# Performance work log

Hardware: AMD Instinct MI355X
Metric: run time of the kernel (lower is better)

Reference implementation:

```python
import jax, jax.numpy as jnp
import numpy as np
jax.config.update("jax_enable_x64", True)  # int64 hash codes for lattice keys

N_KPTS = 32768
C = 61      # feature channels; f-MLP input dim is C+3 = 64
D = 64      # disp-distribution channels
D_LAT = 8   # last f-layer output -> permutohedral position dim

# large odd 62-bit multipliers for the lattice-key hash (wraps mod 2^64)
_MULTS = np.array([2654435761405764093, 1181783497276652981,
                   3202034522624059733, 2685821657736338717,
                   1876998521354586173, 1481765933965188213,
                   2549297995355413921, 3373259426345127233], dtype=np.int64)


def _hcode(k, mults):
    return jnp.sum(k.astype(jnp.int64) * mults, axis=-1)


def _pl_filter(pos, vals):
    """Permutohedral lattice splat -> blur -> slice (approx. Gaussian filter).
    pos: (N, d) float32 lattice positions, vals: (N, vd) float32 values."""
    N, d = pos.shape
    vd = vals.shape[1]
    M = N * (d + 1)  # fixed-size hash table (every point touches d+1 vertices)
    # --- elevate onto hyperplane H_d in R^{d+1} ---
    scale = np.float32(np.sqrt(2.0 / 3.0) * (d + 1)) / np.sqrt(
        np.arange(1, d + 1, dtype=np.float32) * np.arange(2, d + 2, dtype=np.float32))
    E = np.zeros((d + 1, d), dtype=np.float32)
    E[0, :] = 1.0
    for i in range(1, d + 1):
        E[i, i - 1] = -float(i)
        E[i, i:] = 1.0
    elevated = (pos * jnp.asarray(scale, jnp.float32)) @ jnp.asarray(E).T  # (N, d+1)
    # --- nearest zero-colored lattice point and simplex ranks ---
    rem0 = jnp.floor(elevated / (d + 1) + 0.5) * (d + 1)
    sum_val = jnp.round(jnp.sum(rem0, -1) / (d + 1)).astype(jnp.int32)
    diff = elevated - rem0
    rank = jnp.argsort(jnp.argsort(-diff, axis=-1), axis=-1).astype(jnp.int32) + sum_val[:, None]
    lo = rank < 0
    hi = rank > d
    rem0 = rem0 + jnp.where(lo, float(d + 1), 0.0) - jnp.where(hi, float(d + 1), 0.0)
    rank = rank + jnp.where(lo, d + 1, 0) - jnp.where(hi, d + 1, 0)
    # --- barycentric coordinates ---
    t = (elevated - rem0) / (d + 1)
    rows = jnp.arange(N)[:, None]
    bary = jnp.zeros((N, d + 2), jnp.float32)
    bary = bary.at[rows, d - rank].add(t)
    bary = bary.at[rows, d + 1 - rank].add(-t)
    bary = bary.at[:, 0].add(1.0 + bary[:, d + 1])
    w = bary[:, :d + 1]  # (N, d+1) vertex weights
    # --- simplex vertex keys (first d coords; full key sums to 0) ---
    canonical = np.zeros((d + 1, d + 1), np.int32)
    for r in range(d + 1):
        canonical[r, :d + 1 - r] = r
        canonical[r, d + 1 - r:] = r - (d + 1)
    keys = rem0.astype(jnp.int32)[None, :, :d] + jnp.asarray(canonical)[:, rank[:, :d]]  # (d+1,N,d)
    # --- hash table via sorted unique codes (jit-safe fixed size) ---
    mults = jnp.asarray(_MULTS[:d])
    codes = _hcode(keys, mults).reshape(M)
    uniq, inv = jnp.unique(codes, return_inverse=True, size=M,
                           fill_value=jnp.iinfo(jnp.int64).max)
    inv = inv.reshape(M)
    # --- splat ---
    wv = (w.T[:, :, None] * vals[None]).reshape(M, vd)
    lat = jax.ops.segment_sum(wv, inv, num_segments=M)  # (M, vd)
    occ = jax.ops.segment_sum(jnp.ones((M,), jnp.float32), inv, num_segments=M) > 0
    ukeys = jnp.zeros((M, d), jnp.int32).at[inv].set(keys.reshape(M, d))
    # --- blur along each of the d+1 lattice directions ---
    for j in range(d + 1):
        off = np.ones(d + 1, np.int32)
        off[j] = -d
        o = jnp.asarray(off[:d])
        def _nbr(sign, lat=lat):
            c = _hcode(ukeys + sign * o, mults)
            i = jnp.clip(jnp.searchsorted(uniq, c), 0, M - 1)
            ok = (jnp.take(uniq, i) == c) & jnp.take(occ, i)
            return jnp.where(ok[:, None], jnp.take(lat, i, axis=0), 0.0)
        lat = jnp.where(occ[:, None], 0.5 * lat + 0.25 * (_nbr(1) + _nbr(-1)), lat)
    # --- slice ---
    alpha = 1.0 / (1.0 + 2.0 ** (-d))
    return jnp.sum(w.T[:, :, None] * jnp.take(lat, inv, axis=0).reshape(d + 1, N, vd), 0) * alpha


def _layernorm2(x, g, b):
    # LayerNorm(normalized_shape=(N, K)): stats over the last TWO dims jointly
    mu = jnp.mean(x, axis=(-2, -1), keepdims=True)
    var = jnp.mean((x - mu) ** 2, axis=(-2, -1), keepdims=True)
    return (x - mu) * jax.lax.rsqrt(var + 1e-5) * g + b


def setup_inputs() -> dict:
    key = jax.random.key(0)
    ks = jax.random.split(key, 16)
    f32 = jnp.float32
    rn = lambda k, shape, s=1.0: jax.random.normal(k, shape, dtype=f32) * s
    inp = {
        "kpts": rn(ks[0], (1, N_KPTS, 3)),
        "disps_distr": rn(ks[1], (1, N_KPTS, D)),
        "feats": rn(ks[2], (1, N_KPTS, C)),
    }
    i = 3
    for b in range(2):
        inp[f"Wd{b}0"] = rn(ks[i], (D, D), 0.05); i += 1
        inp[f"bd{b}0"] = jnp.zeros((D,), f32)
        inp[f"Wd{b}1"] = rn(ks[i], (D, D), 0.05); i += 1
        inp[f"bd{b}1"] = jnp.zeros((D,), f32)
        inp[f"Wf{b}"] = rn(ks[i], (C + 3, D_LAT), 0.1); i += 1
        inp[f"bf{b}"] = jnp.zeros((D_LAT,), f32)
        inp[f"g{b}"] = jnp.ones((N_KPTS, D_LAT), f32)
        inp[f"be{b}"] = jnp.zeros((N_KPTS, D_LAT), f32)
    return inp


def reference(kpts, disps_distr, feats, Wd00, bd00, Wd01, bd01, Wf0, bf0, g0, be0,
              Wd10, bd10, Wd11, bd11, Wf1, bf1, g1, be1):
    fk = jnp.concatenate([kpts, feats], axis=-1)  # (1, N, C+3)
    x = jnp.reshape(disps_distr, (1, N_KPTS, -1))
    blocks = [(Wd00, bd00, Wd01, bd01, Wf0, bf0, g0, be0),
              (Wd10, bd10, Wd11, bd11, Wf1, bf1, g1, be1)]
    for (Wd0, bd0, Wd1, bd1, Wf, bf, g, be) in blocks:
        x = jax.nn.relu(x @ Wd0 + bd0)   # d-layer 0
        x = jax.nn.relu(x @ Wd1 + bd1)   # d-layer 1
        # only the LAST f-layer output is used by the torch code (feats_kpts is never updated)
        pos = _layernorm2(jax.nn.relu(fk @ Wf + bf), g, be)  # (1, N, 8)
        x = _pl_filter(pos[0], x[0])[None]
    return x
```

## Files before the change

kernel.cpp:

```cpp
#include <hip/hip_runtime.h>
#include <hip/hip_bf16.h>
#include <hip/hip_fp16.h>
#include <stdint.h>

typedef unsigned long long u64;

#define NK 32768
#define DL 8
#define DP1 9
#define MT (NK*DP1)
#define HBITS 20
#define HSIZE (1u<<HBITS)
#define HMASK (HSIZE-1)
#define EMPTY_CODE 0xFFFFFFFFFFFFFFFFULL
#define NBLK 1152
#define HBLK 4096
#define CAP 32

__device__ __constant__ u64 c_mults[8] = {
    2654435761405764093ULL, 1181783497276652981ULL, 3202034522624059733ULL,
    2685821657736338717ULL, 1876998521354586173ULL, 1481765933965188213ULL,
    2549297995355413921ULL, 3373259426345127233ULL};

__device__ __forceinline__ unsigned int hmix(u64 x) {
    x ^= x >> 33; x *= 0xff51afd7ed558ccdULL;
    x ^= x >> 33; x *= 0xc4ceb9fe1a85ec53ULL;
    x ^= x >> 33;
    return (unsigned int)x & HMASK;
}

__device__ __forceinline__ u64 dir_delta(int j) {
    u64 s = 0;
    #pragma unroll
    for (int k = 0; k < 8; k++) s += c_mults[k];
    return (j == 8) ? s : (s - 9ULL * c_mults[j]);
}

__device__ __forceinline__ float ldf(const void* p, int i, int bf) {
    if (bf) return __bfloat162float(((const __hip_bfloat16*)p)[i]);
    return ((const float*)p)[i];
}

__global__ void k_detect(const unsigned* __restrict__ g0w, int* __restrict__ flag) {
    if (threadIdx.x == 0) {
        int f = 1;
        for (int i = 0; i < 8; i++) if (g0w[i] != 0x3F803F80u) f = 0;
        *flag = f;
    }
}

__global__ __launch_bounds__(256) void k_mlp(const void* __restrict__ xin, int use_df_in,
    const void* __restrict__ W0, const void* __restrict__ B0,
    const void* __restrict__ W1, const void* __restrict__ B1,
    float* __restrict__ xout, const int* __restrict__ df, double* __restrict__ stats) {
    __shared__ float w0[64*64], w1[64*64], xs[16][64], y1[16][64];
    int bf = *df;
    int bfin = use_df_in ? bf : 0;
    int tid = threadIdx.x;
    int row0 = blockIdx.x * 16;
    if (blockIdx.x == 0 && tid == 0) { stats[0] = 0.0; stats[1] = 0.0; }
    for (int i = tid; i < 4096; i += 256) { w0[i] = ldf(W0, i, bf); w1[i] = ldf(W1, i, bf); }
    for (int i = tid; i < 1024; i += 256) xs[i>>6][i&63] = ldf(xin, row0*64 + i, bfin);
    __syncthreads();
    int rb = tid >> 6, col = tid & 63;
    float b0c = ldf(B0, col, bf);
    float a0 = b0c, a1 = b0c, a2 = b0c, a3 = b0c;
    #pragma unroll
    for (int k = 0; k < 64; k++) {
        float w = w0[k*64+col];
        a0 = fmaf(xs[rb   ][k], w, a0);
        a1 = fmaf(xs[rb+ 4][k], w, a1);
        a2 = fmaf(xs[rb+ 8][k], w, a2);
        a3 = fmaf(xs[rb+12][k], w, a3);
    }
    y1[rb   ][col] = fmaxf(a0, 0.f);
    y1[rb+ 4][col] = fmaxf(a1, 0.f);
    y1[rb+ 8][col] = fmaxf(a2, 0.f);
    y1[rb+12][col] = fmaxf(a3, 0.f);
    __syncthreads();
    float b1c = ldf(B1, col, bf);
    a0 = b1c; a1 = b1c; a2 = b1c; a3 = b1c;
    #pragma unroll
    for (int k = 0; k < 64; k++) {
        float w = w1[k*64+col];
        a0 = fmaf(y1[rb   ][k], w, a0);
        a1 = fmaf(y1[rb+ 4][k], w, a1);
        a2 = fmaf(y1[rb+ 8][k], w, a2);
        a3 = fmaf(y1[rb+12][k], w, a3);
    }
    xout[(row0+rb   )*64 + col] = fmaxf(a0, 0.f);
    xout[(row0+rb+ 4)*64 + col] = fmaxf(a1, 0.f);
    xout[(row0+rb+ 8)*64 + col] = fmaxf(a2, 0.f);
    xout[(row0+rb+12)*64 + col] = fmaxf(a3, 0.f);
}

__global__ __launch_bounds__(256) void k_pos(const void* __restrict__ kpts,
    const void* __restrict__ feats, const void* __restrict__ Wf,
    const void* __restrict__ Bf, float* __restrict__ pos_pre,
    double* __restrict__ stats, const int* __restrict__ df) {
    __shared__ float wf[64*8];
    __shared__ float fk[32][65];
    __shared__ float red[256], red2[256];
    int bf = *df;
    int tid = threadIdx.x;
    int n0 = blockIdx.x * 32;
    for (int i = tid; i < 512; i += 256) wf[i] = ldf(Wf, i, bf);
    for (int i = tid; i < 32*64; i += 256) {
        int pt = i >> 6, k = i & 63, n = n0 + pt;
        fk[pt][k] = (k < 3) ? ldf(kpts, n*3 + k, bf) : ldf(feats, n*61 + (k-3), bf);
    }
    __syncthreads();
    int pt = tid >> 3, j = tid & 7, n = n0 + pt;
    float acc = ldf(Bf, j, bf);
    #pragma unroll
    for (int k = 0; k < 64; k++) acc = fmaf(fk[pt][k], wf[k*8+j], acc);
    acc = fmaxf(acc, 0.f);
    pos_pre[n*8 + j] = acc;
    red[tid] = acc; red2[tid] = acc * acc;
    __syncthreads();
    for (int s = 128; s > 0; s >>= 1) {
        if (tid < s) { red[tid] += red[tid+s]; red2[tid] += red2[tid+s]; }
        __syncthreads();
    }
    if (tid == 0) { atomicAdd(&stats[0], (double)red[0]); atomicAdd(&stats[1], (double)red2[0]); }
}

__global__ __launch_bounds__(256) void k_embed(const float* __restrict__ pos_pre,
    const double* __restrict__ stats, const void* __restrict__ g,
    const void* __restrict__ be, float* __restrict__ wgt,
    u64* __restrict__ pcodes, int* __restrict__ cnt, const int* __restrict__ df) {
    int bf = *df;
    int n = blockIdx.x * 256 + threadIdx.x;
    if (n >= NK) return;
    const double inv_cnt = 1.0 / (double)(NK * DL);
    double mud = stats[0] * inv_cnt;
    double vard = stats[1] * inv_cnt - mud * mud;
    float mu = (float)mud;
    float rs = rsqrtf((float)vard + 1e-5f);
    const float scale[8] = {
        5.196152422706632f, 3.0f, 2.1213203435596424f, 1.643167672515498f,
        1.3416407864998738f, 1.1338934190276817f, 0.9819805060619657f, 0.8660254037844386f};
    float c[8];
    #pragma unroll
    for (int k = 0; k < 8; k++) {
        float v = pos_pre[n*8 + k];
        float p = (v - mu) * rs * ldf(g, n*8 + k, bf) + ldf(be, n*8 + k, bf);
        c[k] = p * scale[k];
    }
    float sufa[9]; sufa[8] = 0.f;
    #pragma unroll
    for (int k = 7; k >= 0; k--) sufa[k] = sufa[k+1] + c[k];
    float elev[9];
    elev[0] = sufa[0];
    #pragma unroll
    for (int i = 1; i < 9; i++) elev[i] = sufa[i] - (float)i * c[i-1];
    int ri[9], sumv = 0;
    float diff[9];
    #pragma unroll
    for (int i = 0; i < 9; i++) {
        ri[i] = (int)floorf(elev[i] / 9.0f + 0.5f);
        sumv += ri[i];
        diff[i] = elev[i] - 9.f * (float)ri[i];
    }
    int rank[9];
    #pragma unroll
    for (int i = 0; i < 9; i++) {
        int r = 0;
        #pragma unroll
        for (int j = 0; j < 9; j++)
            r += (diff[j] > diff[i]) || ((diff[j] == diff[i]) && (j < i));
        rank[i] = r + sumv;
    }
    #pragma unroll
    for (int i = 0; i < 9; i++) {
        if (rank[i] < 0)      { rank[i] += 9; ri[i] += 1; }
        else if (rank[i] > 8) { rank[i] -= 9; ri[i] -= 1; }
    }
    float t[9];
    #pragma unroll
    for (int i = 0; i < 9; i++) t[i] = (elev[i] - 9.f * (float)ri[i]) / 9.f;
    float bary[10];
    #pragma unroll
    for (int i = 0; i < 10; i++) bary[i] = 0.f;
    #pragma unroll
    for (int i = 0; i < 9; i++) { bary[8 - rank[i]] += t[i]; bary[9 - rank[i]] -= t[i]; }
    bary[0] += 1.f + bary[9];
    for (int r = 0; r < 9; r++) {
        u64 code = 0;
        #pragma unroll
        for (int k = 0; k < 8; k++) {
            int key = 9 * ri[k] + ((rank[k] <= 8 - r) ? r : (r - 9));
            code += (u64)(long long)key * c_mults[k];
        }
        int m = n * 9 + r;
        wgt[m] = bary[r];
        pcodes[m] = code;
        cnt[m] = 0;
    }
}

__global__ __launch_bounds__(256) void k_insert(const u64* __restrict__ pcodes,
    u64* __restrict__ htab_code) {
    int m = blockIdx.x * 256 + threadIdx.x;
    if (m >= MT) return;
    u64 code = pcodes[m];
    unsigned int pos = hmix(code);
    for (;;) {
        u64 cc = htab_code[pos];
        if (cc == code) return;
        if (cc == EMPTY_CODE) {
            u64 old = atomicCAS(&htab_code[pos], EMPTY_CODE, code);
            if (old == EMPTY_CODE || old == code) return;
        }
        pos = (pos + 1) & HMASK;
    }
}

__global__ __launch_bounds__(256) void k_occ(const u64* __restrict__ htab_code,
    int* __restrict__ bocc) {
    __shared__ int wcnt[4];
    unsigned int i = blockIdx.x * 256 + threadIdx.x;
    bool occ = (htab_code[i] != EMPTY_CODE);
    u64 mask = __ballot(occ);
    int lane = threadIdx.x & 63;
    if (lane == 0) wcnt[threadIdx.x >> 6] = __popcll(mask);
    __syncthreads();
    if (threadIdx.x == 0) bocc[blockIdx.x] = wcnt[0] + wcnt[1] + wcnt[2] + wcnt[3];
}

__global__ __launch_bounds__(256) void k_occscan(int* __restrict__ bocc,
    int* __restrict__ counter) {
    __shared__ int s[256];
    __shared__ int carry;
    int t = threadIdx.x;
    if (t == 0) carry = 0;
    __syncthreads();
    for (int c = 0; c < HBLK / 256; c++) {
        int i = c * 256 + t;
        int v = bocc[i];
        s[t] = v; __syncthreads();
        for (int off = 1; off < 256; off <<= 1) {
            int a = (t >= off) ? s[t-off] : 0;
            __syncthreads();
            s[t] += a;
            __syncthreads();
        }
        int cl = carry;
        bocc[i] = s[t] - v + cl;
        __syncthreads();
        if (t == 0) carry = cl + s[255];
        __syncthreads();
    }
    if (t == 0) *counter = carry;
}

__global__ __launch_bounds__(256) void k_assign2(const u64* __restrict__ htab_code,
    const int* __restrict__ bocc, int* __restrict__ htab_slot,
    u64* __restrict__ slot_code) {
    __shared__ int wbase[4];
    unsigned int i = blockIdx.x * 256 + threadIdx.x;
    u64 cde = htab_code[i];
    bool occ = (cde != EMPTY_CODE);
    int lane = threadIdx.x & 63;
    int wid  = threadIdx.x >> 6;
    u64 mask = __ballot(occ);
    int prefix = __popcll(mask & ((1ULL << lane) - 1ULL));
    if (lane == 0) wbase[wid] = __popcll(mask);
    __syncthreads();
    if (threadIdx.x == 0) {
        int run = bocc[blockIdx.x];
        for (int w = 0; w < 4; w++) { int c = wbase[w]; wbase[w] = run; run += c; }
    }
    __syncthreads();
    if (occ) {
        int s = wbase[wid] + prefix;
        htab_slot[i] = s;
        slot_code[s] = cde;
    }
}

__global__ __launch_bounds__(256) void k_nbr(const u64* __restrict__ slot_code,
    const u64* __restrict__ htab_code, const int* __restrict__ htab_slot,
    const int* __restrict__ counter, int2* __restrict__ nbr) {
    int idx = blockIdx.x * 256 + threadIdx.x;
    if (idx >= 9 * MT) return;
    int j = idx / MT;
    int sl = idx - j * MT;
    int count = *counter;
    if (sl >= count) return;
    u64 dj = dir_delta(j);
    u64 code = slot_code[sl];
    int res[2];
    #pragma unroll
    for (int s = 0; s < 2; s++) {
        u64 cde = code + (s ? (u64)(0ULL - dj) : dj);
        unsigned int pos = hmix(cde);
        int r = -1;
        for (;;) {
            u64 cc = htab_code[pos];
            if (cc == cde) { r = htab_slot[pos]; break; }
            if (cc == EMPTY_CODE) break;
            pos = (pos + 1) & HMASK;
        }
        res[s] = r;
    }
    nbr[j * MT + sl] = make_int2(res[0], res[1]);
}

__global__ __launch_bounds__(256) void k_lookup(const u64* __restrict__ pcodes,
    const u64* __restrict__ htab_code, const int* __restrict__ htab_slot,
    int* __restrict__ sidx, int* __restrict__ cnt) {
    int m = blockIdx.x * 256 + threadIdx.x;
    if (m >= MT) return;
    u64 cde = pcodes[m];
    unsigned int pos = hmix(cde);
    while (htab_code[pos] != cde) pos = (pos + 1) & HMASK;
    int s = htab_slot[pos];
    sidx[m] = s;
    atomicAdd(&cnt[s], 1);
}

__global__ __launch_bounds__(256) void k_scan1(const int* __restrict__ cnt,
    int* __restrict__ exbuf, int* __restrict__ bsum) {
    __shared__ int s[256];
    int t = threadIdx.x;
    int i = blockIdx.x * 256 + t;
    int v = cnt[i];
    s[t] = v; __syncthreads();
    for (int off = 1; off < 256; off <<= 1) {
        int a = (t >= off) ? s[t-off] : 0;
        __syncthreads();
        s[t] += a;
        __syncthreads();
    }
    exbuf[i] = s[t] - v;
    if (t == 255) bsum[blockIdx.x] = s[255];
}

__global__ __launch_bounds__(256) void k_scan2(int* __restrict__ bsum) {
    __shared__ int s[256];
    __shared__ int carry;
    int t = threadIdx.x;
    if (t == 0) carry = 0;
    __syncthreads();
    for (int c = 0; c < (NBLK + 255) / 256; c++) {
        int i = c * 256 + t;
        int v = (i < NBLK) ? bsum[i] : 0;
        s[t] = v; __syncthreads();
        for (int off = 1; off < 256; off <<= 1) {
            int a = (t >= off) ? s[t-off] : 0;
            __syncthreads();
            s[t] += a;
            __syncthreads();
        }
        int cl = carry;
        if (i < NBLK) bsum[i] = s[t] - v + cl;
        __syncthreads();
        if (t == 0) carry = cl + s[255];
        __syncthreads();
    }
}

__global__ __launch_bounds__(256) void k_scan3(const int* __restrict__ exbuf,
    const int* __restrict__ bsum, int* __restrict__ start, int* __restrict__ cursor) {
    int i = blockIdx.x * 256 + threadIdx.x;
    int st = exbuf[i] + bsum[blockIdx.x];
    start[i] = st;
    cursor[i] = st;
}

__global__ __launch_bounds__(256) void k_scatter(const int* __restrict__ sidx,
    int* __restrict__ cursor, int* __restrict__ list) {
    int m = blockIdx.x * 256 + threadIdx.x;
    if (m < MT) {
        int pos = atomicAdd(&cursor[sidx[m]], 1);
        list[pos] = m;
    }
}

__global__ __launch_bounds__(256) void k_splat_a(const float* __restrict__ xbuf,
    const float* __restrict__ wgt, const int* __restrict__ start,
    const int* __restrict__ cnt, const int* __restrict__ list,
    float* __restrict__ val, const int* __restrict__ counter) {
    int count = *counter;
    int sl = blockIdx.x * 8 + (threadIdx.x >> 5);
    int lane = threadIdx.x & 31;
    if (sl >= count) return;
    int c = cnt[sl], st = start[sl];
    const float2* x2 = (const float2*)xbuf;
    float2 acc = make_float2(0.f, 0.f);
    if (c <= CAP) {
        int mm = 0; float ww = 0.f;
        if (lane < c) { mm = list[st + lane]; ww = wgt[mm]; }
        for (int k = 0; k < c; k++) {
            int   m = __shfl(mm, k, 32);
            float w = __shfl(ww, k, 32);
            float2 xv = x2[(m / 9) * 32 + lane];
            acc.x = fmaf(w, xv.x, acc.x);
            acc.y = fmaf(w, xv.y, acc.y);
        }
    }
    ((float2*)val)[(size_t)sl * 32 + lane] = acc;
}

__global__ __launch_bounds__(256) void k_splat_b(const float* __restrict__ xbuf,
    const float* __restrict__ wgt, const int* __restrict__ sidx,
    const int* __restrict__ cnt, const int* __restrict__ list,
    float* __restrict__ val) {
    int chunk = blockIdx.x * 8 + (threadIdx.x >> 5);
    int lane = threadIdx.x & 31;
    int e = chunk * 32 + lane;
    int m = 0, slot = -1; float w = 0.f; int hub = 0;
    if (e < MT) {
        m = list[e];
        slot = sidx[m];
        hub = (cnt[slot] > CAP);
        if (hub) w = wgt[m];
    }
    u64 bal = __ballot(hub);
    unsigned int half = (threadIdx.x & 32) ? (unsigned int)(bal >> 32) : (unsigned int)bal;
    if (!half) return;
    const float2* x2 = (const float2*)xbuf;
    float2 acc = make_float2(0.f, 0.f);
    int cur = -1;
    while (half) {
        int k = __ffs(half) - 1; half &= half - 1;
        int   sk = __shfl(slot, k, 32);
        int   mk = __shfl(m, k, 32);
        float wk = __shfl(w, k, 32);
        float2 xv = x2[(mk / 9) * 32 + lane];
        if (sk != cur) {
            if (cur >= 0) {
                atomicAdd(&val[(size_t)cur * 64 + 2*lane    ], acc.x);
                atomicAdd(&val[(size_t)cur * 64 + 2*lane + 1], acc.y);
            }
            cur = sk; acc = make_float2(0.f, 0.f);
        }
        acc.x = fmaf(wk, xv.x, acc.x);
        acc.y = fmaf(wk, xv.y, acc.y);
    }
    atomicAdd(&val[(size_t)cur * 64 + 2*lane    ], acc.x);
    atomicAdd(&val[(size_t)cur * 64 + 2*lane + 1], acc.y);
}

__global__ __launch_bounds__(256) void k_blur0(const float* __restrict__ vin,
    __half* __restrict__ vout, const int2* __restrict__ nbrj,
    const int* __restrict__ counter) {
    int idx = blockIdx.x * 256 + threadIdx.x;
    int sl = idx >> 4, la = idx & 15;
    int count = *counter;
    if (sl >= count) return;
    int2 nbp = nbrj[sl];
    const float4* vin4 = (const float4*)vin;
    float4 S = vin4[(size_t)sl*16 + la];
    float4 z = make_float4(0.f,0.f,0.f,0.f);
    float4 A = (nbp.x >= 0) ? vin4[(size_t)nbp.x*16 + la] : z;
    float4 B = (nbp.y >= 0) ? vin4[(size_t)nbp.y*16 + la] : z;
    float4 o;
    o.x = 0.5f*S.x + 0.25f*(A.x + B.x);
    o.y = 0.5f*S.y + 0.25f*(A.y + B.y);
    o.z = 0.5f*S.z + 0.25f*(A.z + B.z);
    o.w = 0.5f*S.w + 0.25f*(A.w + B.w);
    union { __half2 h; unsigned u; } h0, h1;
    h0.h = __float22half2_rn(make_float2(o.x, o.y));
    h1.h = __float22half2_rn(make_float2(o.z, o.w));
    ((uint2*)vout)[(size_t)sl*16 + la] = make_uint2(h0.u, h1.u);
}

__global__ __launch_bounds__(256) void k_blur(const __half* __restrict__ vin,
    __half* __restrict__ vout, const int2* __restrict__ nbrj,
    const int* __restrict__ counter) {
    int idx = blockIdx.x * 256 + threadIdx.x;
    int sl = idx >> 3, lane = idx & 7;
    int count = *counter;
    if (sl >= count) return;
    int2 nbp = nbrj[sl];
    typedef union { uint4 u; __half2 h[4]; } row16;
    const uint4* vin4 = (const uint4*)vin;
    uint4* vout4 = (uint4*)vout;
    row16 S, A, B, O;
    S.u = vin4[(size_t)sl*8 + lane];
    uint4 z; z.x = 0; z.y = 0; z.z = 0; z.w = 0;
    A.u = (nbp.x >= 0) ? vin4[(size_t)nbp.x*8 + lane] : z;
    B.u = (nbp.y >= 0) ? vin4[(size_t)nbp.y*8 + lane] : z;
    #pragma unroll
    for (int k = 0; k < 4; k++) {
        float2 fs = __half22float2(S.h[k]);
        float2 fa = __half22float2(A.h[k]);
        float2 fb = __half22float2(B.h[k]);
        float2 r;
        r.x = 0.5f * fs.x + 0.25f * (fa.x + fb.x);
        r.y = 0.5f * fs.y + 0.25f * (fa.y + fb.y);
        O.h[k] = __float22half2_rn(r);
    }
    vout4[(size_t)sl*8 + lane] = O.u;
}

__global__ __launch_bounds__(256) void k_slice(const float* __restrict__ wgt,
    const int* __restrict__ sidx, const __half* __restrict__ val,
    float* __restrict__ outf, void* __restrict__ outb, int write_out,
    const int* __restrict__ df) {
    int bf = *df;
    int idx = blockIdx.x * 256 + threadIdx.x;
    if (idx >= NK * 64) return;
    int n = idx >> 6, ch = idx & 63;
    float acc = 0.f;
    #pragma unroll
    for (int r = 0; r < 9; r++) {
        int m = n * 9 + r;
        acc = fmaf(wgt[m], __half2float(val[(size_t)sidx[m]*64 + ch]), acc);
    }
    acc *= 0.9961089494163424f;
    if (write_out) {
        if (bf) ((__hip_bfloat16*)outb)[idx] = __float2bfloat16(acc);
        else    ((float*)outb)[idx] = acc;
    } else {
        outf[idx] = acc;
    }
}

extern "C" void kernel_launch(void* const* d_in, const int* in_sizes, int n_in,
                              void* d_out, int out_size, void* d_ws, size_t ws_size,
                              hipStream_t stream) {
    const void* kpts  = d_in[0];
    const void* disps = d_in[1];
    const void* feats = d_in[2];

    char* p = (char*)d_ws;
    float* xbuf     = (float*)p;  p += (size_t)NK*64*4;
    float* pos_pre  = (float*)p;  p += (size_t)NK*8*4;
    double* stats   = (double*)p; p += 256;
    int*   dflag    = (int*)p;    p += 256;
    float* wgt      = (float*)p;  p += (size_t)MT*4;
    int*   sidx     = (int*)p;    p += (size_t)MT*4;
    u64*   pcodes   = (u64*)p;    p += (size_t)MT*8;
    u64*   htabc    = (u64*)p;    p += (size_t)HSIZE*8;
    int*   htabs    = (int*)p;    p += (size_t)HSIZE*4;
    u64*   slotc    = (u64*)p;    p += (size_t)MT*8;
    int*   counter  = (int*)p;    p += 256;
    int*   bocc     = (int*)p;    p += (size_t)HBLK*4;
    int*   cnt      = (int*)p;    p += (size_t)MT*4;
    int*   exbuf    = (int*)p;    p += (size_t)MT*4;
    int*   startA   = (int*)p;    p += (size_t)MT*4;
    int*   cursor   = (int*)p;    p += (size_t)MT*4;
    int*   list     = (int*)p;    p += (size_t)MT*4;
    int*   bsum     = (int*)p;    p += 256*32;
    int2*  nbr      = (int2*)p;   p += (size_t)MT*9*8;
    float*  val0    = (float*)p;  p += (size_t)MT*64*4;
    __half* val1    = (__half*)p; p += (size_t)MT*64*2;
    __half* val2    = (__half*)p; p += (size_t)MT*64*2;

    k_detect<<<1, 64, 0, stream>>>((const unsigned*)d_in[3 + 6], dflag);

    for (int b = 0; b < 2; b++) {
        const void* W0 = d_in[3 + b*8 + 0];
        const void* B0 = d_in[3 + b*8 + 1];
        const void* W1 = d_in[3 + b*8 + 2];
        const void* B1 = d_in[3 + b*8 + 3];
        const void* Wf = d_in[3 + b*8 + 4];
        const void* Bf = d_in[3 + b*8 + 5];
        const void* G  = d_in[3 + b*8 + 6];
        const void* Be = d_in[3 + b*8 + 7];

        k_mlp<<<NK/16, 256, 0, stream>>>(b == 0 ? disps : (const void*)xbuf, b == 0 ? 1 : 0,
                                         W0, B0, W1, B1, xbuf, dflag, stats);

        k_pos<<<NK/32, 256, 0, stream>>>(kpts, feats, Wf, Bf, pos_pre, stats, dflag);

        hipMemsetAsync(htabc, 0xFF, (size_t)HSIZE*8, stream);

        k_embed<<<NK/256, 256, 0, stream>>>(pos_pre, stats, G, Be, wgt, pcodes, cnt, dflag);
        k_insert<<<NBLK, 256, 0, stream>>>(pcodes, htabc);
        k_occ<<<HBLK, 256, 0, stream>>>(htabc, bocc);
        k_occscan<<<1, 256, 0, stream>>>(bocc, counter);
        k_assign2<<<HBLK, 256, 0, stream>>>(htabc, bocc, htabs, slotc);
        k_nbr<<<(9*MT + 255)/256, 256, 0, stream>>>(slotc, htabc, htabs, counter, nbr);
        k_lookup<<<NBLK, 256, 0, stream>>>(pcodes, htabc, htabs, sidx, cnt);

        k_scan1<<<NBLK, 256, 0, stream>>>(cnt, exbuf, bsum);
        k_scan2<<<1, 256, 0, stream>>>(bsum);
        k_scan3<<<NBLK, 256, 0, stream>>>(exbuf, bsum, startA, cursor);
        k_scatter<<<NBLK, 256, 0, stream>>>(sidx, cursor, list);
        k_splat_a<<<(MT + 7)/8, 256, 0, stream>>>(xbuf, wgt, startA, cnt, list, val0, counter);
        k_splat_b<<<(MT/32 + 7)/8, 256, 0, stream>>>(xbuf, wgt, sidx, cnt, list, val0);

        k_blur0<<<(MT*16 + 255)/256, 256, 0, stream>>>(val0, val1, nbr + 0*MT, counter);
        for (int j = 1; j < 9; j++) {
            const __half* vin = (j & 1) ? val1 : val2;
            __half*       vout = (j & 1) ? val2 : val1;
            k_blur<<<(MT*8 + 255)/256, 256, 0, stream>>>(vin, vout, nbr + (size_t)j*MT, counter);
        }
        k_slice<<<(NK*64)/256, 256, 0, stream>>>(wgt, sidx, val1, xbuf,
                                                 d_out, b == 1 ? 1 : 0, dflag);
    }
}
```

Measured before the change: 801.6 us.

## Splat directly to fp16, replace atomic hub splat with block reduction, shrink hash

```diff
diff --git a/kernel.cpp b/kernel.cpp
--- a/kernel.cpp
+++ b/kernel.cpp
@@ -9,13 +9,14 @@
 #define DL 8
 #define DP1 9
 #define MT (NK*DP1)
-#define HBITS 20
+#define HBITS 19
 #define HSIZE (1u<<HBITS)
 #define HMASK (HSIZE-1)
 #define EMPTY_CODE 0xFFFFFFFFFFFFFFFFULL
 #define NBLK 1152
-#define HBLK 4096
+#define HBLK (HSIZE/256)
 #define CAP 32
+#define MAXHUB 16384
 
 __device__ __constant__ u64 c_mults[8] = {
     2654435761405764093ULL, 1181783497276652981ULL, 3202034522624059733ULL,
@@ -229,11 +230,11 @@
 }
 
 __global__ __launch_bounds__(256) void k_occscan(int* __restrict__ bocc,
-    int* __restrict__ counter) {
+    int* __restrict__ counter, int* __restrict__ nhub) {
     __shared__ int s[256];
     __shared__ int carry;
     int t = threadIdx.x;
-    if (t == 0) carry = 0;
+    if (t == 0) { carry = 0; *nhub = 0; }
     __syncthreads();
     for (int c = 0; c < HBLK / 256; c++) {
         int i = c * 256 + t;
@@ -321,11 +322,13 @@
 }
 
 __global__ __launch_bounds__(256) void k_scan1(const int* __restrict__ cnt,
-    int* __restrict__ exbuf, int* __restrict__ bsum) {
+    int* __restrict__ exbuf, int* __restrict__ bsum,
+    int* __restrict__ hublist, int* __restrict__ nhub) {
     __shared__ int s[256];
     int t = threadIdx.x;
     int i = blockIdx.x * 256 + t;
     int v = cnt[i];
+    if (v > CAP) { int h = atomicAdd(nhub, 1); if (h < MAXHUB) hublist[h] = i; }
     s[t] = v; __syncthreads();
     for (int off = 1; off < 256; off <<= 1) {
         int a = (t >= off) ? s[t-off] : 0;
@@ -381,90 +384,58 @@
 __global__ __launch_bounds__(256) void k_splat_a(const float* __restrict__ xbuf,
     const float* __restrict__ wgt, const int* __restrict__ start,
     const int* __restrict__ cnt, const int* __restrict__ list,
-    float* __restrict__ val, const int* __restrict__ counter) {
+    __half* __restrict__ val, const int* __restrict__ counter) {
     int count = *counter;
     int sl = blockIdx.x * 8 + (threadIdx.x >> 5);
     int lane = threadIdx.x & 31;
     if (sl >= count) return;
-    int c = cnt[sl], st = start[sl];
+    int c = cnt[sl];
+    if (c > CAP) return;
+    int st = start[sl];
     const float2* x2 = (const float2*)xbuf;
     float2 acc = make_float2(0.f, 0.f);
-    if (c <= CAP) {
-        int mm = 0; float ww = 0.f;
-        if (lane < c) { mm = list[st + lane]; ww = wgt[mm]; }
-        for (int k = 0; k < c; k++) {
-            int   m = __shfl(mm, k, 32);
-            float w = __shfl(ww, k, 32);
+    int mm = 0; float ww = 0.f;
+    if (lane < c) { mm = list[st + lane]; ww = wgt[mm]; }
+    for (int k = 0; k < c; k++) {
+        int   m = __shfl(mm, k, 32);
+        float w = __shfl(ww, k, 32);
+        float2 xv = x2[(m / 9) * 32 + lane];
+        acc.x = fmaf(w, xv.x, acc.x);
+        acc.y = fmaf(w, xv.y, acc.y);
+    }
+    ((__half2*)val)[(size_t)sl * 32 + lane] = __float22half2_rn(acc);
+}
+
+__global__ __launch_bounds__(256) void k_splat_hub(const float* __restrict__ xbuf,
+    const float* __restrict__ wgt, const int* __restrict__ start,
+    const int* __restrict__ cnt, const int* __restrict__ list,
+    const int* __restrict__ hublist, const int* __restrict__ nhub,
+    __half* __restrict__ val) {
+    __shared__ float2 red[8][32];
+    int nh = *nhub;
+    int grp = threadIdx.x >> 5, lane = threadIdx.x & 31;
+    const float2* x2 = (const float2*)xbuf;
+    for (int hi = blockIdx.x; hi < nh; hi += gridDim.x) {
+        int sl = hublist[hi];
+        int st = start[sl], c = cnt[sl];
+        float2 acc = make_float2(0.f, 0.f);
+        for (int k = grp; k < c; k += 8) {
+            int m = list[st + k];
+            float w = wgt[m];
             float2 xv = x2[(m / 9) * 32 + lane];
             acc.x = fmaf(w, xv.x, acc.x);
             acc.y = fmaf(w, xv.y, acc.y);
         }
-    }
-    ((float2*)val)[(size_t)sl * 32 + lane] = acc;
-}
-
-__global__ __launch_bounds__(256) void k_splat_b(const float* __restrict__ xbuf,
-    const float* __restrict__ wgt, const int* __restrict__ sidx,
-    const int* __restrict__ cnt, const int* __restrict__ list,
-    float* __restrict__ val) {
-    int chunk = blockIdx.x * 8 + (threadIdx.x >> 5);
-    int lane = threadIdx.x & 31;
-    int e = chunk * 32 + lane;
-    int m = 0, slot = -1; float w = 0.f; int hub = 0;
-    if (e < MT) {
-        m = list[e];
-        slot = sidx[m];
-        hub = (cnt[slot] > CAP);
-        if (hub) w = wgt[m];
-    }
-    u64 bal = __ballot(hub);
-    unsigned int half = (threadIdx.x & 32) ? (unsigned int)(bal >> 32) : (unsigned int)bal;
-    if (!half) return;
-    const float2* x2 = (const float2*)xbuf;
-    float2 acc = make_float2(0.f, 0.f);
-    int cur = -1;
-    while (half) {
-        int k = __ffs(half) - 1; half &= half - 1;
-        int   sk = __shfl(slot, k, 32);
-        int   mk = __shfl(m, k, 32);
-        float wk = __shfl(w, k, 32);
-        float2 xv = x2[(mk / 9) * 32 + lane];
-        if (sk != cur) {
-            if (cur >= 0) {
-                atomicAdd(&val[(size_t)cur * 64 + 2*lane    ], acc.x);
-                atomicAdd(&val[(size_t)cur * 64 + 2*lane + 1], acc.y);
-            }
-            cur = sk; acc = make_float2(0.f, 0.f);
-        }
-        acc.x = fmaf(wk, xv.x, acc.x);
-        acc.y = fmaf(wk, xv.y, acc.y);
-    }
-    atomicAdd(&val[(size_t)cur * 64 + 2*lane    ], acc.x);
-    atomicAdd(&val[(size_t)cur * 64 + 2*lane + 1], acc.y);
-}
-
-__global__ __launch_bounds__(256) void k_blur0(const float* __restrict__ vin,
-    __half* __restrict__ vout, const int2* __restrict__ nbrj,
-    const int* __restrict__ counter) {
-    int idx = blockIdx.x * 256 + threadIdx.x;
-    int sl = idx >> 4, la = idx & 15;
-    int count = *counter;
-    if (sl >= count) return;
-    int2 nbp = nbrj[sl];
-    const float4* vin4 = (const float4*)vin;
-    float4 S = vin4[(size_t)sl*16 + la];
-    float4 z = make_float4(0.f,0.f,0.f,0.f);
-    float4 A = (nbp.x >= 0) ? vin4[(size_t)nbp.x*16 + la] : z;
-    float4 B = (nbp.y >= 0) ? vin4[(size_t)nbp.y*16 + la] : z;
-    float4 o;
-    o.x = 0.5f*S.x + 0.25f*(A.x + B.x);
-    o.y = 0.5f*S.y + 0.25f*(A.y + B.y);
-    o.z = 0.5f*S.z + 0.25f*(A.z + B.z);
-    o.w = 0.5f*S.w + 0.25f*(A.w + B.w);
-    union { __half2 h; unsigned u; } h0, h1;
-    h0.h = __float22half2_rn(make_float2(o.x, o.y));
-    h1.h = __float22half2_rn(make_float2(o.z, o.w));
-    ((uint2*)vout)[(size_t)sl*16 + la] = make_uint2(h0.u, h1.u);
+        red[grp][lane] = acc;
+        __syncthreads();
+        if (grp == 0) {
+            float2 s = red[0][lane];
+            #pragma unroll
+            for (int g = 1; g < 8; g++) { s.x += red[g][lane].x; s.y += red[g][lane].y; }
+            ((__half2*)val)[(size_t)sl * 32 + lane] = __float22half2_rn(s);
+        }
+        __syncthreads();
+    }
 }
 
 __global__ __launch_bounds__(256) void k_blur(const __half* __restrict__ vin,
@@ -538,6 +509,7 @@
     int*   htabs    = (int*)p;    p += (size_t)HSIZE*4;
     u64*   slotc    = (u64*)p;    p += (size_t)MT*8;
     int*   counter  = (int*)p;    p += 256;
+    int*   nhub     = (int*)p;    p += 256;
     int*   bocc     = (int*)p;    p += (size_t)HBLK*4;
     int*   cnt      = (int*)p;    p += (size_t)MT*4;
     int*   exbuf    = (int*)p;    p += (size_t)MT*4;
@@ -545,10 +517,10 @@
     int*   cursor   = (int*)p;    p += (size_t)MT*4;
     int*   list     = (int*)p;    p += (size_t)MT*4;
     int*   bsum     = (int*)p;    p += 256*32;
+    int*   hublist  = (int*)p;    p += (size_t)MAXHUB*4;
     int2*  nbr      = (int2*)p;   p += (size_t)MT*9*8;
-    float*  val0    = (float*)p;  p += (size_t)MT*64*4;
-    __half* val1    = (__half*)p; p += (size_t)MT*64*2;
-    __half* val2    = (__half*)p; p += (size_t)MT*64*2;
+    __half* valA    = (__half*)p; p += (size_t)MT*64*2;
+    __half* valB    = (__half*)p; p += (size_t)MT*64*2;
 
     k_detect<<<1, 64, 0, stream>>>((const unsigned*)d_in[3 + 6], dflag);
 
@@ -572,25 +544,24 @@
         k_embed<<<NK/256, 256, 0, stream>>>(pos_pre, stats, G, Be, wgt, pcodes, cnt, dflag);
         k_insert<<<NBLK, 256, 0, stream>>>(pcodes, htabc);
         k_occ<<<HBLK, 256, 0, stream>>>(htabc, bocc);
-        k_occscan<<<1, 256, 0, stream>>>(bocc, counter);
+        k_occscan<<<1, 256, 0, stream>>>(bocc, counter, nhub);
         k_assign2<<<HBLK, 256, 0, stream>>>(htabc, bocc, htabs, slotc);
         k_nbr<<<(9*MT + 255)/256, 256, 0, stream>>>(slotc, htabc, htabs, counter, nbr);
         k_lookup<<<NBLK, 256, 0, stream>>>(pcodes, htabc, htabs, sidx, cnt);
 
-        k_scan1<<<NBLK, 256, 0, stream>>>(cnt, exbuf, bsum);
+        k_scan1<<<NBLK, 256, 0, stream>>>(cnt, exbuf, bsum, hublist, nhub);
         k_scan2<<<1, 256, 0, stream>>>(bsum);
         k_scan3<<<NBLK, 256, 0, stream>>>(exbuf, bsum, startA, cursor);
         k_scatter<<<NBLK, 256, 0, stream>>>(sidx, cursor, list);
-        k_splat_a<<<(MT + 7)/8, 256, 0, stream>>>(xbuf, wgt, startA, cnt, list, val0, counter);
-        k_splat_b<<<(MT/32 + 7)/8, 256, 0, stream>>>(xbuf, wgt, sidx, cnt, list, val0);
-
-        k_blur0<<<(MT*16 + 255)/256, 256, 0, stream>>>(val0, val1, nbr + 0*MT, counter);
-        for (int j = 1; j < 9; j++) {
-            const __half* vin = (j & 1) ? val1 : val2;
-            __half*       vout = (j & 1) ? val2 : val1;
+        k_splat_a<<<(MT + 7)/8, 256, 0, stream>>>(xbuf, wgt, startA, cnt, list, valA, counter);
+        k_splat_hub<<<512, 256, 0, stream>>>(xbuf, wgt, startA, cnt, list, hublist, nhub, valA);
+
+        for (int j = 0; j < 9; j++) {
+            const __half* vin = (j & 1) ? valB : valA;
+            __half*       vout = (j & 1) ? valA : valB;
             k_blur<<<(MT*8 + 255)/256, 256, 0, stream>>>(vin, vout, nbr + (size_t)j*MT, counter);
         }
-        k_slice<<<(NK*64)/256, 256, 0, stream>>>(wgt, sidx, val1, xbuf,
+        k_slice<<<(NK*64)/256, 256, 0, stream>>>(wgt, sidx, valB, xbuf,
                                                  d_out, b == 1 ? 1 : 0, dflag);
     }
 }
```

Result: slower. 972.1 us (+21.3%).
